# Optimization experiments

Measured on AMD Instinct MI355X. Metric: run time of the kernel, lower is better.

## Reference

```python
import jax, jax.numpy as jnp
import numpy as np

B, N, C = 16, 196608, 2

def setup_inputs() -> dict:
    key = jax.random.key(0)
    k1, k2, k3, k4, k5 = jax.random.split(key, 5)
    return {
        "r": jax.random.normal(k1, (B, N, C), dtype=jnp.float32),
        "w": jax.random.uniform(k2, (B, N, 2), dtype=jnp.float32),
        "J_p": jax.random.normal(k3, (B, N, C, 6), dtype=jnp.float32),
        "J_d": jax.random.uniform(k4, (B, N, C, 1), dtype=jnp.float32),
        "lmbda": jax.random.uniform(k5, (B, 1, 1), dtype=jnp.float32),
    }

def reference(r, w, J_p, J_d, lmbda):
    # r: (B,N,C)  w: (B,N,2)  J_p: (B,N,C,6)  J_d: (B,N,C,1)  lmbda: (B,1,1)
    conf = w[..., 0:1]                                  # (B,N,1)
    node_lambda = w[..., 1:2]                           # (B,N,1)
    conf4 = conf[..., None]                             # (B,N,1,1)
    Jd = J_d[..., 0]                                    # (B,N,C)

    # Gauss-Newton blocks (sum-over-N reductions of tiny outer products)
    H_pp = jnp.einsum('bnki,bnkj->bij', J_p, conf4 * J_p)        # (B,6,6)
    H_pd = jnp.einsum('bnki,bnkj->bnij', J_p, conf4 * J_d)       # (B,N,6,1)
    H_dd = jnp.einsum('bnk,bnk->bn', Jd, conf * Jd)[..., None]   # (B,N,1)
    wr = conf * r                                                # (B,N,C)
    g_p = jnp.einsum('bnki,bnk->bi', J_p, wr)[..., None]         # (B,6,1)
    g_d = jnp.einsum('bnk,bnk->bn', Jd, wr)[..., None]           # (B,N,1)

    eye6 = jnp.eye(6, dtype=H_pp.dtype)[None]                    # (1,6,6)
    H_pp = H_pp + lmbda * eye6                                   # LM damping on pose block

    # Depth block damping + safe inverse
    H_dd_safe = jnp.maximum(H_dd + lmbda + node_lambda, 1e-4)    # (B,N,1)
    inv_H_dd = 1.0 / H_dd_safe                                   # (B,N,1)

    # Schur complement: H_eff = H_pp - sum_n H_pd invHdd H_pd^T
    H_pd_invHdd = H_pd * inv_H_dd[..., None]                     # (B,N,6,1)
    term = jnp.einsum('bnik,bnjk->bij', H_pd_invHdd, H_pd)       # (B,6,6)
    H_eff = H_pp - term + (0.01 + 0.001) * eye6                  # eye*0.01 then ridge 0.001
    g_eff = g_p - jnp.sum(H_pd_invHdd * g_d[..., None], axis=1)  # (B,6,1)

    delta_pose = jnp.linalg.solve(H_eff, g_eff)                  # (B,6,1)
    dp = delta_pose[..., 0]                                      # (B,6)

    # Back-substitute depths
    v = jnp.einsum('bnij,bi->bnj', H_pd, dp)                     # (B,N,1)
    delta_depth = inv_H_dd * (g_d - v)                           # (B,N,1)

    delta_pose_out = jnp.clip(dp, -2.0, 2.0)                     # (B,6)
    return (delta_pose_out, delta_depth)
```

## Files before the change

### kernel.cpp

```cpp
#include <hip/hip_runtime.h>


using f4 = __attribute__((ext_vector_type(4))) float;
using f2 = __attribute__((ext_vector_type(2))) float;

__device__ __forceinline__ f4 ntload4(const f4* p) {
    return __builtin_nontemporal_load(p);
}

constexpr int NACC = 27;

__device__ __forceinline__ void accum_point(
    const float ja[6], const float jb[6],
    float r0, float r1, float conf, float nlam, float jd0, float jd1,
    float lam, float* __restrict__ A, float* __restrict__ g,
    float* __restrict__ c7)
{
    float h[6], gp[6];
#pragma unroll
    for (int i = 0; i < 6; ++i) {
        h[i]  = conf * (ja[i] * jd0 + jb[i] * jd1);
        gp[i] = conf * (ja[i] * r0 + jb[i] * r1);
    }
    const float hdd = conf * (jd0 * jd0 + jd1 * jd1);
    const float inv = 1.0f / fmaxf(hdd + lam + nlam, 1e-4f);
    const float gd  = conf * (jd0 * r0 + jd1 * r1);
    const float gdinv = gd * inv;
    c7[6] = gdinv;
    int idx = 0;
#pragma unroll
    for (int i = 0; i < 6; ++i) {
        const float hii = h[i] * inv;
        c7[i] = hii;
#pragma unroll
        for (int j = i; j < 6; ++j) {
            A[idx] += conf * (ja[i] * ja[j] + jb[i] * jb[j]) - hii * h[j];
            ++idx;
        }
        g[i] += gp[i] - h[i] * gdinv;
    }
}

__device__ __forceinline__ void solve6(const float* __restrict__ a, float lam,
                                       float* __restrict__ pose,
                                       float* __restrict__ dp)
{
    float M[6][7];
    int idx = 0;
#pragma unroll
    for (int i = 0; i < 6; ++i) {
#pragma unroll
        for (int j = i; j < 6; ++j) {
            const float t = a[idx++];
            M[i][j] = t;
            M[j][i] = t;
        }
    }
#pragma unroll
    for (int i = 0; i < 6; ++i) M[i][6] = a[21 + i];
#pragma unroll
    for (int i = 0; i < 6; ++i) M[i][i] += lam + 0.011f;
#pragma unroll
    for (int k = 0; k < 6; ++k) {
        const float piv = 1.0f / M[k][k];
#pragma unroll
        for (int j = 0; j < 7; ++j) M[k][j] *= piv;
#pragma unroll
        for (int i = 0; i < 6; ++i) {
            if (i == k) continue;
            const float f = M[i][k];
#pragma unroll
            for (int j = 0; j < 7; ++j) M[i][j] -= f * M[k][j];
        }
    }
#pragma unroll
    for (int i = 0; i < 6; ++i) {
        const float x = M[i][6];
        dp[i] = x;
        pose[i] = fminf(fmaxf(x, -2.0f), 2.0f);
    }
}

__global__ __launch_bounds__(256) void dba_reduce_swz(
    const float* __restrict__ r, const float* __restrict__ w,
    const float* __restrict__ J_p, const float* __restrict__ J_d,
    const float* __restrict__ lmbda, float* __restrict__ acc,
    float* __restrict__ cA, float* __restrict__ cB, float* __restrict__ cC,
    int N)
{
    const int b = blockIdx.y;
    const float lam = lmbda[b];
    const int lane = threadIdx.x & 63;
    const int wave = threadIdx.x >> 6;

    const size_t basePt = (size_t)b * (size_t)N;
    const int P = N >> 1;
    const f4* __restrict__ r4  = (const f4*)r   + (basePt >> 1);
    const f4* __restrict__ w4  = (const f4*)w   + (basePt >> 1);
    const f4* __restrict__ jd4 = (const f4*)J_d + (basePt >> 1);
    const f4* __restrict__ jp4 = (const f4*)J_p + basePt * 3;
    f4* __restrict__ cA4 = (f4*)cA + basePt;
    f4* __restrict__ cB4 = (f4*)cB + (basePt >> 1);
    f2* __restrict__ cC2 = (f2*)cC + (basePt >> 1);

    const int chunksPerXcd = (P >> 6) >> 3;
    const int wavesPerXcd  = (gridDim.x >> 3) << 2;
    const int cpw  = chunksPerXcd / wavesPerXcd;
    const int xcd  = blockIdx.x & 7;
    const int wslot = ((blockIdx.x >> 3) << 2) + wave;
    const int c0 = xcd * chunksPerXcd + wslot * cpw;

    float A[21];
    float g[6];
#pragma unroll
    for (int i = 0; i < 21; ++i) A[i] = 0.f;
#pragma unroll
    for (int i = 0; i < 6; ++i) g[i] = 0.f;

    for (int c = c0; c < c0 + cpw; ++c) {
        const int pr = (c << 6) + lane;
        const f4 rv = ntload4(r4 + pr);
        const f4 wv = ntload4(w4 + pr);
        const f4 jd = ntload4(jd4 + pr);
        const f4* jp = jp4 + (size_t)pr * 6;
        const f4 q0 = ntload4(jp + 0);
        const f4 q1 = ntload4(jp + 1);
        const f4 q2 = ntload4(jp + 2);
        const f4 q3 = ntload4(jp + 3);
        const f4 q4 = ntload4(jp + 4);
        const f4 q5 = ntload4(jp + 5);

        float c7a[7], c7b[7];
        {
            const float ja[6] = {q0[0], q0[1], q0[2], q0[3], q1[0], q1[1]};
            const float jb[6] = {q1[2], q1[3], q2[0], q2[1], q2[2], q2[3]};
            accum_point(ja, jb, rv[0], rv[1], wv[0], wv[1], jd[0], jd[1],
                        lam, A, g, c7a);
        }
        {
            const float ja[6] = {q3[0], q3[1], q3[2], q3[3], q4[0], q4[1]};
            const float jb[6] = {q4[2], q4[3], q5[0], q5[1], q5[2], q5[3]};
            accum_point(ja, jb, rv[2], rv[3], wv[2], wv[3], jd[2], jd[3],
                        lam, A, g, c7b);
        }
        const size_t pt = (size_t)pr << 1;
        f4 a0 = {c7a[0], c7a[1], c7a[2], c7a[3]};
        f4 a1 = {c7b[0], c7b[1], c7b[2], c7b[3]};
        f4 bq = {c7a[4], c7a[5], c7b[4], c7b[5]};
        f2 cq = {c7a[6], c7b[6]};
        cA4[pt]     = a0;
        cA4[pt + 1] = a1;
        cB4[pr]     = bq;
        cC2[pr]     = cq;
    }

    float v[NACC];
#pragma unroll
    for (int i = 0; i < 21; ++i) v[i] = A[i];
#pragma unroll
    for (int i = 0; i < 6; ++i) v[21 + i] = g[i];
#pragma unroll
    for (int off = 32; off > 0; off >>= 1) {
#pragma unroll
        for (int i = 0; i < NACC; ++i) v[i] += __shfl_down(v[i], off, 64);
    }
    __shared__ float sred[4][NACC];
    if (lane == 0) {
#pragma unroll
        for (int i = 0; i < NACC; ++i) sred[wave][i] = v[i];
    }
    __syncthreads();
    if (threadIdx.x < NACC) {
        const float s = sred[0][threadIdx.x] + sred[1][threadIdx.x] +
                        sred[2][threadIdx.x] + sred[3][threadIdx.x];
        atomicAdd(&acc[b * 32 + threadIdx.x], s);
    }
}

__global__ void dba_solve(const float* __restrict__ acc,
                          const float* __restrict__ lmbda,
                          float* __restrict__ pose_out,
                          float* __restrict__ dp_ws, int B)
{
    const int b = blockIdx.x * blockDim.x + threadIdx.x;
    if (b >= B) return;
    solve6(acc + b * 32, lmbda[b], pose_out + b * 6, dp_ws + b * 6);
}

__global__ __launch_bounds__(256) void dba_depth_swz(
    const float* __restrict__ cA, const float* __restrict__ cB,
    const float* __restrict__ cC, const float* __restrict__ dp_ws,
    float* __restrict__ depth_out, int N)
{
    const int b = blockIdx.y;
    float dp[6];
#pragma unroll
    for (int i = 0; i < 6; ++i) dp[i] = dp_ws[b * 6 + i];

    const size_t basePt = (size_t)b * (size_t)N;
    const int P = N >> 1;
    const f4* __restrict__ cA4 = (const f4*)cA + basePt;
    const f4* __restrict__ cB4 = (const f4*)cB + (basePt >> 1);
    const f2* __restrict__ cC2 = (const f2*)cC + (basePt >> 1);
    f2* __restrict__ out2 = (f2*)depth_out + (basePt >> 1);

    const int lane = threadIdx.x & 63;
    const int wave = threadIdx.x >> 6;
    const int pairsPerXcd   = P >> 3;
    const int pairsPerBlock = pairsPerXcd / (gridDim.x >> 3);
    const int perWave = pairsPerBlock >> 2;
    const int xcd = blockIdx.x & 7;
    const int base = xcd * pairsPerXcd + (blockIdx.x >> 3) * pairsPerBlock +
                     wave * perWave;

    for (int i = 0; i < perWave; i += 64) {
        const int pr = base + i + lane;
        const size_t pt = (size_t)pr << 1;
        const f4 a0 = cA4[pt];
        const f4 a1 = cA4[pt + 1];
        const f4 bq = cB4[pr];
        const f2 cq = cC2[pr];
        f2 o;
        o[0] = cq[0] - (a0[0] * dp[0] + a0[1] * dp[1] + a0[2] * dp[2] +
                        a0[3] * dp[3] + bq[0] * dp[4] + bq[1] * dp[5]);
        o[1] = cq[1] - (a1[0] * dp[0] + a1[1] * dp[1] + a1[2] * dp[2] +
                        a1[3] * dp[3] + bq[2] * dp[4] + bq[3] * dp[5]);
        __builtin_nontemporal_store(o, out2 + pr);
    }
}

__global__ __launch_bounds__(256) void dba_reduce_fb(
    const float* __restrict__ r, const float* __restrict__ w,
    const float* __restrict__ J_p, const float* __restrict__ J_d,
    const float* __restrict__ lmbda, float* __restrict__ acc, int N)
{
    const int b = blockIdx.y;
    const float lam = lmbda[b];
    float A[21];
    float g[6];
#pragma unroll
    for (int i = 0; i < 21; ++i) A[i] = 0.f;
#pragma unroll
    for (int i = 0; i < 6; ++i) g[i] = 0.f;

    const size_t basePt = (size_t)b * (size_t)N;
    const int P = N >> 1;
    const f4* __restrict__ r4  = (const f4*)r   + (basePt >> 1);
    const f4* __restrict__ w4  = (const f4*)w   + (basePt >> 1);
    const f4* __restrict__ jd4 = (const f4*)J_d + (basePt >> 1);
    const f4* __restrict__ jp4 = (const f4*)J_p + basePt * 3;

    float c7a[7], c7b[7];
    for (int pr = blockIdx.x * blockDim.x + threadIdx.x; pr < P;
         pr += gridDim.x * blockDim.x) {
        const f4 rv = r4[pr];
        const f4 wv = w4[pr];
        const f4 jd = jd4[pr];
        const f4* jp = jp4 + (size_t)pr * 6;
        const f4 q0 = jp[0], q1 = jp[1], q2 = jp[2];
        const f4 q3 = jp[3], q4 = jp[4], q5 = jp[5];
        {
            const float ja[6] = {q0[0], q0[1], q0[2], q0[3], q1[0], q1[1]};
            const float jb[6] = {q1[2], q1[3], q2[0], q2[1], q2[2], q2[3]};
            accum_point(ja, jb, rv[0], rv[1], wv[0], wv[1], jd[0], jd[1],
                        lam, A, g, c7a);
        }
        {
            const float ja[6] = {q3[0], q3[1], q3[2], q3[3], q4[0], q4[1]};
            const float jb[6] = {q4[2], q4[3], q5[0], q5[1], q5[2], q5[3]};
            accum_point(ja, jb, rv[2], rv[3], wv[2], wv[3], jd[2], jd[3],
                        lam, A, g, c7b);
        }
    }

    float v[NACC];
#pragma unroll
    for (int i = 0; i < 21; ++i) v[i] = A[i];
#pragma unroll
    for (int i = 0; i < 6; ++i) v[21 + i] = g[i];
#pragma unroll
    for (int off = 32; off > 0; off >>= 1) {
#pragma unroll
        for (int i = 0; i < NACC; ++i) v[i] += __shfl_down(v[i], off, 64);
    }
    __shared__ float sred[4][NACC];
    const int wave = threadIdx.x >> 6;
    const int lane = threadIdx.x & 63;
    if (lane == 0) {
#pragma unroll
        for (int i = 0; i < NACC; ++i) sred[wave][i] = v[i];
    }
    __syncthreads();
    if (threadIdx.x < NACC) {
        const float s = sred[0][threadIdx.x] + sred[1][threadIdx.x] +
                        sred[2][threadIdx.x] + sred[3][threadIdx.x];
        atomicAdd(&acc[b * 32 + threadIdx.x], s);
    }
}

__global__ __launch_bounds__(256) void dba_depth_fb(
    const float* __restrict__ r, const float* __restrict__ w,
    const float* __restrict__ J_p, const float* __restrict__ J_d,
    const float* __restrict__ lmbda, const float* __restrict__ dp_ws,
    float* __restrict__ depth_out, int N)
{
    const int b = blockIdx.y;
    const float lam = lmbda[b];
    float dp[6];
#pragma unroll
    for (int i = 0; i < 6; ++i) dp[i] = dp_ws[b * 6 + i];

    const size_t basePt = (size_t)b * (size_t)N;
    const int P = N >> 1;
    const f4* __restrict__ r4  = (const f4*)r   + (basePt >> 1);
    const f4* __restrict__ w4  = (const f4*)w   + (basePt >> 1);
    const f4* __restrict__ jd4 = (const f4*)J_d + (basePt >> 1);
    const f4* __restrict__ jp4 = (const f4*)J_p + basePt * 3;
    f2* __restrict__ out2 = (f2*)depth_out + (basePt >> 1);

    for (int pr = blockIdx.x * blockDim.x + threadIdx.x; pr < P;
         pr += gridDim.x * blockDim.x) {
        const f4 rv = r4[pr];
        const f4 wv = w4[pr];
        const f4 jd = jd4[pr];
        const f4* jp = jp4 + (size_t)pr * 6;
        const f4 q0 = jp[0], q1 = jp[1], q2 = jp[2];
        const f4 q3 = jp[3], q4 = jp[4], q5 = jp[5];
        f2 o;
        {
            const float ja[6] = {q0[0], q0[1], q0[2], q0[3], q1[0], q1[1]};
            const float jb[6] = {q1[2], q1[3], q2[0], q2[1], q2[2], q2[3]};
            float v = 0.f;
#pragma unroll
            for (int i = 0; i < 6; ++i)
                v += (ja[i] * jd[0] + jb[i] * jd[1]) * dp[i];
            v *= wv[0];
            const float hdd = wv[0] * (jd[0] * jd[0] + jd[1] * jd[1]);
            const float inv = 1.0f / fmaxf(hdd + lam + wv[1], 1e-4f);
            const float gd  = wv[0] * (jd[0] * rv[0] + jd[1] * rv[1]);
            o[0] = inv * (gd - v);
        }
        {
            const float ja[6] = {q3[0], q3[1], q3[2], q3[3], q4[0], q4[1]};
            const float jb[6] = {q4[2], q4[3], q5[0], q5[1], q5[2], q5[3]};
            float v = 0.f;
#pragma unroll
            for (int i = 0; i < 6; ++i)
                v += (ja[i] * jd[2] + jb[i] * jd[3]) * dp[i];
            v *= wv[2];
            const float hdd = wv[2] * (jd[2] * jd[2] + jd[3] * jd[3]);
            const float inv = 1.0f / fmaxf(hdd + lam + wv[3], 1e-4f);
            const float gd  = wv[2] * (jd[2] * rv[2] + jd[3] * rv[3]);
            o[1] = inv * (gd - v);
        }
        out2[pr] = o;
    }
}

extern "C" void kernel_launch(void* const* d_in, const int* in_sizes, int n_in,
                              void* d_out, int out_size, void* d_ws, size_t ws_size,
                              hipStream_t stream)
{
    const float* r   = (const float*)d_in[0];
    const float* w   = (const float*)d_in[1];
    const float* J_p = (const float*)d_in[2];
    const float* J_d = (const float*)d_in[3];
    const float* lmb = (const float*)d_in[4];
    const int B = in_sizes[4];
    const int N = in_sizes[0] / (B * 2);

    float* acc   = (float*)d_ws;
    float* dp_ws = (float*)d_ws + 512;
    float* cA    = (float*)d_ws + 1024;
    float* cB    = cA + (size_t)B * N * 4;
    float* cC    = cB + (size_t)B * N * 2;
    float* out   = (float*)d_out;
    float* pose  = out;
    float* depth = out + B * 6;

    const size_t cacheBytes = (size_t)B * (size_t)N * 28;
    const bool fast = (B == 16) && (N == 196608) &&
                      (ws_size >= 4096 + cacheBytes);

    hipMemsetAsync(acc, 0, B * 32 * sizeof(float), stream);

    if (fast) {
        dim3 rgrid(64, B);
        dba_reduce_swz<<<rgrid, 256, 0, stream>>>(r, w, J_p, J_d, lmb, acc,
                                                  cA, cB, cC, N);
        dba_solve<<<1, 64, 0, stream>>>(acc, lmb, pose, dp_ws, B);
        dim3 dgrid(128, B);
        dba_depth_swz<<<dgrid, 256, 0, stream>>>(cA, cB, cC, dp_ws, depth, N);
    } else {
        dim3 grid(192, B);
        dba_reduce_fb<<<grid, 256, 0, stream>>>(r, w, J_p, J_d, lmb, acc, N);
        dba_solve<<<1, 64, 0, stream>>>(acc, lmb, pose, dp_ws, B);
        dba_depth_fb<<<grid, 256, 0, stream>>>(r, w, J_p, J_d, lmb, dp_ws,
                                               depth, N);
    }
}
```

Measured before the change: 312.2 us.

## Software-prefetch next chunk in reduce and depth loops, double reduce grid

```diff
diff --git a/kernel.cpp b/kernel.cpp
--- a/kernel.cpp
+++ b/kernel.cpp
@@ -3,10 +3,6 @@
 
 using f4 = __attribute__((ext_vector_type(4))) float;
 using f2 = __attribute__((ext_vector_type(2))) float;
-
-__device__ __forceinline__ f4 ntload4(const f4* p) {
-    return __builtin_nontemporal_load(p);
-}
 
 constexpr int NACC = 27;
 
@@ -81,7 +77,7 @@
     }
 }
 
-__global__ __launch_bounds__(256) void dba_reduce_swz(
+__global__ __launch_bounds__(256, 2) void dba_reduce_swz(
     const float* __restrict__ r, const float* __restrict__ w,
     const float* __restrict__ J_p, const float* __restrict__ J_d,
     const float* __restrict__ lmbda, float* __restrict__ acc,
@@ -117,41 +113,62 @@
 #pragma unroll
     for (int i = 0; i < 6; ++i) g[i] = 0.f;
 
-    for (int c = c0; c < c0 + cpw; ++c) {
-        const int pr = (c << 6) + lane;
-        const f4 rv = ntload4(r4 + pr);
-        const f4 wv = ntload4(w4 + pr);
-        const f4 jd = ntload4(jd4 + pr);
-        const f4* jp = jp4 + (size_t)pr * 6;
-        const f4 q0 = ntload4(jp + 0);
-        const f4 q1 = ntload4(jp + 1);
-        const f4 q2 = ntload4(jp + 2);
-        const f4 q3 = ntload4(jp + 3);
-        const f4 q4 = ntload4(jp + 4);
-        const f4 q5 = ntload4(jp + 5);
+    int c = c0;
+    int pr = (c << 6) + lane;
+    f4 c_rv = r4[pr];
+    f4 c_wv = w4[pr];
+    f4 c_jd = jd4[pr];
+    const f4* jpc = jp4 + (size_t)pr * 6;
+    f4 c_q0 = jpc[0];
+    f4 c_q1 = jpc[1];
+    f4 c_q2 = jpc[2];
+    f4 c_q3 = jpc[3];
+    f4 c_q4 = jpc[4];
+    f4 c_q5 = jpc[5];
+
+    for (int i = 0; i < cpw; ++i) {
+        const int cn  = (i + 1 < cpw) ? c + 1 : c;
+        const int prn = (cn << 6) + lane;
+        f4 n_rv = r4[prn];
+        f4 n_wv = w4[prn];
+        f4 n_jd = jd4[prn];
+        const f4* jpn = jp4 + (size_t)prn * 6;
+        f4 n_q0 = jpn[0];
+        f4 n_q1 = jpn[1];
+        f4 n_q2 = jpn[2];
+        f4 n_q3 = jpn[3];
+        f4 n_q4 = jpn[4];
+        f4 n_q5 = jpn[5];
 
         float c7a[7], c7b[7];
         {
-            const float ja[6] = {q0[0], q0[1], q0[2], q0[3], q1[0], q1[1]};
-            const float jb[6] = {q1[2], q1[3], q2[0], q2[1], q2[2], q2[3]};
-            accum_point(ja, jb, rv[0], rv[1], wv[0], wv[1], jd[0], jd[1],
-                        lam, A, g, c7a);
-        }
-        {
-            const float ja[6] = {q3[0], q3[1], q3[2], q3[3], q4[0], q4[1]};
-            const float jb[6] = {q4[2], q4[3], q5[0], q5[1], q5[2], q5[3]};
-            accum_point(ja, jb, rv[2], rv[3], wv[2], wv[3], jd[2], jd[3],
-                        lam, A, g, c7b);
-        }
-        const size_t pt = (size_t)pr << 1;
-        f4 a0 = {c7a[0], c7a[1], c7a[2], c7a[3]};
-        f4 a1 = {c7b[0], c7b[1], c7b[2], c7b[3]};
-        f4 bq = {c7a[4], c7a[5], c7b[4], c7b[5]};
-        f2 cq = {c7a[6], c7b[6]};
-        cA4[pt]     = a0;
-        cA4[pt + 1] = a1;
-        cB4[pr]     = bq;
-        cC2[pr]     = cq;
+            const float ja[6] = {c_q0[0], c_q0[1], c_q0[2], c_q0[3], c_q1[0], c_q1[1]};
+            const float jb[6] = {c_q1[2], c_q1[3], c_q2[0], c_q2[1], c_q2[2], c_q2[3]};
+            accum_point(ja, jb, c_rv[0], c_rv[1], c_wv[0], c_wv[1],
+                        c_jd[0], c_jd[1], lam, A, g, c7a);
+        }
+        {
+            const float ja[6] = {c_q3[0], c_q3[1], c_q3[2], c_q3[3], c_q4[0], c_q4[1]};
+            const float jb[6] = {c_q4[2], c_q4[3], c_q5[0], c_q5[1], c_q5[2], c_q5[3]};
+            accum_point(ja, jb, c_rv[2], c_rv[3], c_wv[2], c_wv[3],
+                        c_jd[2], c_jd[3], lam, A, g, c7b);
+        }
+        {
+            const size_t pt = (size_t)pr << 1;
+            f4 a0 = {c7a[0], c7a[1], c7a[2], c7a[3]};
+            f4 a1 = {c7b[0], c7b[1], c7b[2], c7b[3]};
+            f4 bq = {c7a[4], c7a[5], c7b[4], c7b[5]};
+            f2 cq = {c7a[6], c7b[6]};
+            cA4[pt]     = a0;
+            cA4[pt + 1] = a1;
+            cB4[pr]     = bq;
+            cC2[pr]     = cq;
+        }
+
+        c_rv = n_rv; c_wv = n_wv; c_jd = n_jd;
+        c_q0 = n_q0; c_q1 = n_q1; c_q2 = n_q2;
+        c_q3 = n_q3; c_q4 = n_q4; c_q5 = n_q5;
+        c = cn; pr = prn;
     }
 
     float v[NACC];
@@ -209,23 +226,33 @@
     const int pairsPerXcd   = P >> 3;
     const int pairsPerBlock = pairsPerXcd / (gridDim.x >> 3);
     const int perWave = pairsPerBlock >> 2;
+    const int iters = perWave >> 6;
     const int xcd = blockIdx.x & 7;
     const int base = xcd * pairsPerXcd + (blockIdx.x >> 3) * pairsPerBlock +
                      wave * perWave;
 
-    for (int i = 0; i < perWave; i += 64) {
-        const int pr = base + i + lane;
-        const size_t pt = (size_t)pr << 1;
-        const f4 a0 = cA4[pt];
-        const f4 a1 = cA4[pt + 1];
-        const f4 bq = cB4[pr];
-        const f2 cq = cC2[pr];
+    int pr = base + lane;
+    f4 a0 = cA4[(size_t)pr << 1];
+    f4 a1 = cA4[((size_t)pr << 1) + 1];
+    f4 bq = cB4[pr];
+    f2 cq = cC2[pr];
+
+    for (int i = 0; i < iters; ++i) {
+        const int prn = (i + 1 < iters) ? pr + 64 : pr;
+        f4 na0 = cA4[(size_t)prn << 1];
+        f4 na1 = cA4[((size_t)prn << 1) + 1];
+        f4 nbq = cB4[prn];
+        f2 ncq = cC2[prn];
+
         f2 o;
         o[0] = cq[0] - (a0[0] * dp[0] + a0[1] * dp[1] + a0[2] * dp[2] +
                         a0[3] * dp[3] + bq[0] * dp[4] + bq[1] * dp[5]);
         o[1] = cq[1] - (a1[0] * dp[0] + a1[1] * dp[1] + a1[2] * dp[2] +
                         a1[3] * dp[3] + bq[2] * dp[4] + bq[3] * dp[5]);
         __builtin_nontemporal_store(o, out2 + pr);
+
+        a0 = na0; a1 = na1; bq = nbq; cq = ncq;
+        pr = prn;
     }
 }
 
@@ -385,7 +412,7 @@
     hipMemsetAsync(acc, 0, B * 32 * sizeof(float), stream);
 
     if (fast) {
-        dim3 rgrid(64, B);
+        dim3 rgrid(128, B);
         dba_reduce_swz<<<rgrid, 256, 0, stream>>>(r, w, J_p, J_d, lmb, acc,
                                                   cA, cB, cC, N);
         dba_solve<<<1, 64, 0, stream>>>(acc, lmb, pose, dp_ws, B);
```

Result: faster. 306.0 us (-2.0%).
